# Performance work log

Measured on AMD Instinct MI355X. Metric: run time of the kernel, lower is better.

Reference implementation:

```python
import jax, jax.numpy as jnp
import numpy as np

K = 16            # neighbors
QUERY_CHUNK = 256 # SE is applied per chunk of this many query points (matches torch loop)
EPS = 1e-5        # BatchNorm eps (eval mode, running stats)


def bn(x, g, b, m, v):
    # eval-mode batchnorm over last axis (channel-last layout here)
    return (x - m) * (g / jnp.sqrt(v + EPS)) + b


def setup_inputs() -> dict:
    key = jax.random.key(0)
    ks = jax.random.split(key, 16)
    B, Cin, N = 4, 128, 4096
    H, Cout = 128, 256
    se_h = Cout // 4
    r = lambda k, s, sc=1.0: jax.random.normal(k, s, jnp.float32) * sc
    return dict(
        x=r(ks[0], (B, Cin, N)),
        W_edge=r(ks[1], (H, 2 * Cin), 0.05),          # edge_mlp conv2d 1x1
        bn1_g=jnp.ones((H,), jnp.float32), bn1_b=jnp.zeros((H,), jnp.float32),
        bn1_m=r(ks[2], (H,), 0.1), bn1_v=jax.random.uniform(ks[3], (H,), jnp.float32) + 0.5,
        w_att=r(ks[4], (H,), 0.1),                     # att_conv (1,H,1,1)
        W_fuse=r(ks[5], (Cout, H), 0.05),              # fuse conv1d
        bn2_g=jnp.ones((Cout,), jnp.float32), bn2_b=jnp.zeros((Cout,), jnp.float32),
        bn2_m=r(ks[6], (Cout,), 0.1), bn2_v=jax.random.uniform(ks[7], (Cout,), jnp.float32) + 0.5,
        fc1_w=r(ks[8], (se_h, Cout), 0.05), fc1_b=jnp.zeros((se_h,), jnp.float32),
        fc2_w=r(ks[9], (Cout, se_h), 0.05), fc2_b=jnp.zeros((Cout,), jnp.float32),
        W_res=r(ks[10], (Cout, Cin), 0.05),            # res_conv conv1d (in!=out)
        bn3_g=jnp.ones((Cout,), jnp.float32), bn3_b=jnp.zeros((Cout,), jnp.float32),
        bn3_m=r(ks[11], (Cout,), 0.1), bn3_v=jax.random.uniform(ks[12], (Cout,), jnp.float32) + 0.5,
    )


def reference(x, W_edge, bn1_g, bn1_b, bn1_m, bn1_v, w_att,
              W_fuse, bn2_g, bn2_b, bn2_m, bn2_v,
              fc1_w, fc1_b, fc2_w, fc2_b,
              W_res, bn3_g, bn3_b, bn3_m, bn3_v):
    B, Cin, N = x.shape
    x_t = jnp.swapaxes(x, 1, 2)  # (B,N,Cin)

    # KNN on features (dynamic=False -> knn on x.transpose); squared euclidean
    # has the same ordering as torch.cdist(p=2).
    sq = jnp.sum(x_t * x_t, axis=-1)                               # (B,N)
    d2 = sq[:, :, None] + sq[:, None, :] - 2.0 * jnp.einsum('bnc,bmc->bnm', x_t, x_t)
    _, idx = jax.lax.top_k(-d2, K)                                  # (B,N,K) smallest dists

    neigh = jax.vmap(lambda p, i: p[i])(x_t, idx)                   # (B,N,K,Cin)
    center = jnp.broadcast_to(x_t[:, :, None, :], neigh.shape)      # (B,N,K,Cin)
    edge = jnp.concatenate([neigh - center, center], axis=-1)       # (B,N,K,2Cin)

    # edge_mlp: 1x1 conv + BN + ReLU
    h = jax.nn.relu(bn(jnp.einsum('bnkc,hc->bnkh', edge, W_edge),
                       bn1_g, bn1_b, bn1_m, bn1_v))                 # (B,N,K,H)

    # attention over neighbors
    att = jax.nn.softmax(jnp.einsum('bnkh,h->bnk', h, w_att), axis=-1)
    agg = jnp.einsum('bnkh,bnk->bnh', h, att)                       # (B,N,H)

    # fuse conv1d + BN + ReLU
    out = jax.nn.relu(bn(jnp.einsum('bnh,oh->bno', agg, W_fuse),
                         bn2_g, bn2_b, bn2_m, bn2_v))               # (B,N,Cout)

    # SE channel attention, applied per query chunk (matches torch loop semantics)
    Cout = out.shape[-1]
    nc = N // QUERY_CHUNK
    oc = out.reshape(B, nc, QUERY_CHUNK, Cout)
    s = oc.mean(axis=2)                                             # (B,nc,Cout)
    s = jax.nn.relu(jnp.einsum('bmc,hc->bmh', s, fc1_w) + fc1_b)
    s = jax.nn.sigmoid(jnp.einsum('bmh,ch->bmc', s, fc2_w) + fc2_b)
    out = (oc * s[:, :, None, :]).reshape(B, N, Cout)

    # residual projection (in_channels != out_channels)
    res = bn(jnp.einsum('bnc,oc->bno', x_t, W_res), bn3_g, bn3_b, bn3_m, bn3_v)
    out = out + res
    return jnp.swapaxes(out, 1, 2)                                  # (B,Cout,N)
```

## Files before the change

### kernel.cpp

```cpp
#include <hip/hip_runtime.h>
#include <cstddef>

typedef __bf16 bf16;
typedef __bf16 bf16x8 __attribute__((ext_vector_type(8)));
typedef float  f32x4  __attribute__((ext_vector_type(4)));
typedef unsigned short u16;
typedef unsigned long long u64;

#define MFMA16x16(a, b, c) __builtin_amdgcn_mfma_f32_16x16x32_bf16((a), (b), (c), 0, 0, 0)

namespace {
constexpr int BB   = 4;
constexpr int CIN  = 128;
constexpr int NPT  = 4096;
constexpr int KNBR = 16;
constexpr int HED  = 128;
constexpr int COUT = 256;
}

__device__ __forceinline__ double mk_keyd(float d, unsigned mlo ) {
  const u64 k = ((u64)__float_as_uint(d) << 32) | mlo;
  return __longlong_as_double((long long)k);
}
__device__ __forceinline__ int key_idx(double kd) {
  return (int)((__double_as_longlong(kd) >> 20) & 0xFFF);
}

__device__ __forceinline__ void sort16d(double* k) {
  #pragma unroll
  for (int sz = 2; sz <= 16; sz <<= 1) {
    #pragma unroll
    for (int st = sz >> 1; st > 0; st >>= 1) {
      #pragma unroll
      for (int i = 0; i < 16; ++i) {
        const int j = i ^ st;
        if (j > i) {
          const bool up = ((i & sz) == 0);
          const double a = k[i], c = k[j];
          const double lo = fmin(a, c), hi = fmax(a, c);
          k[i] = up ? lo : hi;
          k[j] = up ? hi : lo;
        }
      }
    }
  }
}

__device__ __forceinline__ void merge16d(double* R, const double* B) {
  double t[16];
  #pragma unroll
  for (int i = 0; i < 16; ++i) t[i] = fmin(R[i], B[15 - i]);
  #pragma unroll
  for (int st = 8; st > 0; st >>= 1) {
    #pragma unroll
    for (int i = 0; i < 16; ++i) {
      const int j = i ^ st;
      if (j > i) {
        const double a = t[i], c = t[j];
        t[i] = fmin(a, c);
        t[j] = fmax(a, c);
      }
    }
  }
  #pragma unroll
  for (int i = 0; i < 16; ++i) R[i] = t[i];
}

__device__ __forceinline__ void shfl_merge16d(double* R, int mask) {
  double B[16];
  #pragma unroll
  for (int i = 0; i < 16; ++i) B[i] = __shfl_xor(R[i], mask, 64);
  merge16d(R, B);
}

__global__ __launch_bounds__(256) void k_wconv(const float* __restrict__ We,
                                               const float* __restrict__ Wf,
                                               const float* __restrict__ Wr,
                                               bf16* __restrict__ Web,
                                               bf16* __restrict__ Wfb,
                                               bf16* __restrict__ Wrb) {
  const int i = blockIdx.x * 256 + threadIdx.x;
  const int a = i >> 15;
  const int j = i & 32767;
  const float* src = (a == 0) ? We : (a == 1) ? Wf : Wr;
  bf16*        dst = (a == 0) ? Web : (a == 1) ? Wfb : Wrb;
  dst[j] = (bf16)src[j];
}

__global__ __launch_bounds__(256) void k_prep(const float* __restrict__ x,
                                              bf16* __restrict__ xh,
                                              bf16* __restrict__ xl,
                                              float* __restrict__ sq) {
  __shared__ __attribute__((aligned(16))) bf16 th[64][136];
  __shared__ __attribute__((aligned(16))) bf16 tl[64][136];
  __shared__ float sqp[4][64];
  const int tid = threadIdx.x;
  const int b   = blockIdx.x >> 6;
  const int n0  = (blockIdx.x & 63) << 6;
  const int nl  = tid & 63;
  const int cg  = tid >> 6;
  const float* xb = x + (size_t)b * CIN * NPT;
  float acc = 0.f;
  #pragma unroll
  for (int rep = 0; rep < 32; ++rep) {
    const int c = rep * 4 + cg;
    const float v = xb[(size_t)c * NPT + n0 + nl];
    const bf16 h = (bf16)v;
    const bf16 l = (bf16)(v - (float)h);
    acc += v * v;
    th[nl][c] = h;
    tl[nl][c] = l;
  }
  sqp[cg][nl] = acc;
  __syncthreads();
  bf16* xho = xh + ((size_t)b * NPT + n0) * CIN;
  bf16* xlo = xl + ((size_t)b * NPT + n0) * CIN;
  #pragma unroll
  for (int rep = 0; rep < 32; ++rep) {
    const int e = rep * 256 + tid;
    const int r = e >> 7;
    const int c = e & 127;
    xho[(size_t)r * CIN + c] = th[r][c];
    xlo[(size_t)r * CIN + c] = tl[r][c];
  }
  if (tid < 64) {
    sq[b * NPT + n0 + tid] = sqp[0][tid] + sqp[1][tid] + sqp[2][tid] + sqp[3][tid];
  }
}

__global__ __launch_bounds__(256, 2) void k_knn(const bf16* __restrict__ xh,
                                                const bf16* __restrict__ xl,
                                                const float* __restrict__ sq,
                                                int* __restrict__ knn_idx) {
  __shared__ double Lk[32][66];
  const int tid  = threadIdx.x;
  const int w    = tid >> 6;
  const int lane = tid & 63;
  const int col  = lane & 15;
  const int quad = lane >> 4;
  const int b    = blockIdx.x >> 7;
  const int q0   = (blockIdx.x & 127) << 5;
  const bf16*  xhb = xh + (size_t)b * NPT * CIN;
  const bf16*  xlb = xl + (size_t)b * NPT * CIN;
  const float* sqb = sq + b * NPT;

  bf16x8 qh[2][4], ql[2][4];
  float sqn[2];
  #pragma unroll
  for (int t = 0; t < 2; ++t) {
    const bf16* qrh = xhb + (size_t)(q0 + t * 16 + col) * CIN + quad * 8;
    const bf16* qrl = xlb + (size_t)(q0 + t * 16 + col) * CIN + quad * 8;
    #pragma unroll
    for (int ks = 0; ks < 4; ++ks) {
      qh[t][ks] = *(const bf16x8*)(qrh + ks * 32);
      ql[t][ks] = *(const bf16x8*)(qrl + ks * 32);
    }
    sqn[t] = sqb[q0 + t * 16 + col];
  }

  const double INF = __builtin_inf();
  double R0[16], R1[16];
  #pragma unroll
  for (int i = 0; i < 16; ++i) { R0[i] = INF; R1[i] = INF; }

  const int cbase = w << 10;
  for (int mt = 0; mt < 16; ++mt) {
    const int m0 = cbase + (mt << 6);
    double k0[16], k1[16];
    #pragma unroll
    for (int cb = 0; cb < 4; ++cb) {
      const bf16* crh = xhb + (size_t)(m0 + cb * 16 + col) * CIN + quad * 8;
      const bf16* crl = xlb + (size_t)(m0 + cb * 16 + col) * CIN + quad * 8;
      f32x4 a0 = {0.f, 0.f, 0.f, 0.f};
      f32x4 a1 = {0.f, 0.f, 0.f, 0.f};
      #pragma unroll
      for (int ks = 0; ks < 4; ++ks) {
        const bf16x8 ch_ = *(const bf16x8*)(crh + ks * 32);
        const bf16x8 cl_ = *(const bf16x8*)(crl + ks * 32);
        a0 = MFMA16x16(cl_, qh[0][ks], a0);
        a0 = MFMA16x16(ch_, ql[0][ks], a0);
        a0 = MFMA16x16(ch_, qh[0][ks], a0);
        a1 = MFMA16x16(cl_, qh[1][ks], a1);
        a1 = MFMA16x16(ch_, ql[1][ks], a1);
        a1 = MFMA16x16(ch_, qh[1][ks], a1);
      }
      const f32x4 sqm = *(const f32x4*)(sqb + m0 + cb * 16 + quad * 4);
      const unsigned mlo0 = (unsigned)(m0 + cb * 16 + quad * 4) << 20;
      #pragma unroll
      for (int r = 0; r < 4; ++r) {
        k0[cb * 4 + r] = mk_keyd((sqn[0] + sqm[r]) - 2.0f * a0[r], mlo0 + ((unsigned)r << 20));
        k1[cb * 4 + r] = mk_keyd((sqn[1] + sqm[r]) - 2.0f * a1[r], mlo0 + ((unsigned)r << 20));
      }
    }
    sort16d(k0); merge16d(R0, k0);
    sort16d(k1); merge16d(R1, k1);
  }

  shfl_merge16d(R0, 16);
  shfl_merge16d(R0, 32);
  shfl_merge16d(R1, 16);
  shfl_merge16d(R1, 32);

  if (quad == 0) {
    #pragma unroll
    for (int i = 0; i < 16; ++i) {
      Lk[col][w * 16 + i]        = R0[i];
      Lk[16 | col][w * 16 + i]   = R1[i];
    }
  }
  __syncthreads();

  if (tid < 64) {
    const int q = tid >> 1;
    const int j = tid & 1;
    double A[16], Bv[16];
    #pragma unroll
    for (int i = 0; i < 16; ++i) {
      A[i]  = Lk[q][(2 * j) * 16 + i];
      Bv[i] = Lk[q][(2 * j + 1) * 16 + i];
    }
    merge16d(A, Bv);
    #pragma unroll
    for (int i = 0; i < 16; ++i) Lk[q][j * 16 + i] = A[i];
  }
  __syncthreads();
  if (tid < 32) {
    double A[16], Bv[16];
    #pragma unroll
    for (int i = 0; i < 16; ++i) {
      A[i]  = Lk[tid][i];
      Bv[i] = Lk[tid][16 + i];
    }
    merge16d(A, Bv);
    int* op = knn_idx + (size_t)(b * NPT + q0 + tid) * KNBR;
    #pragma unroll
    for (int i = 0; i < 16; ++i) op[i] = key_idx(A[i]);
  }
}

__global__ __launch_bounds__(256) void k_edge(const bf16* __restrict__ xh,
                                              const bf16* __restrict__ xl,
                                              const int* __restrict__ knn_idx,
                                              const bf16* __restrict__ We,
                                              const float* __restrict__ g1, const float* __restrict__ b1,
                                              const float* __restrict__ m1, const float* __restrict__ v1,
                                              const float* __restrict__ watt,
                                              bf16* __restrict__ agg) {
  __shared__ __attribute__((aligned(16))) bf16 Ew[4][16][264];
  __shared__ float s1[HED], t1[HED], wat[HED];
  const int tid  = threadIdx.x;
  const int w    = tid >> 6;
  const int lane = tid & 63;
  const int col  = lane & 15;
  const int quad = lane >> 4;
  if (tid < HED) {
    const float ss = g1[tid] / sqrtf(v1[tid] + 1e-5f);
    s1[tid] = ss;
    t1[tid] = b1[tid] - m1[tid] * ss;
    wat[tid] = watt[tid];
  }
  __syncthreads();
  const int gw = blockIdx.x * 4 + w;
  for (int it = 0; it < 4; ++it) {
    const int p = gw * 4 + it;
    const int b = p >> 12;
    const int n = p & 4095;
    const bf16* xhb = xh + (size_t)b * NPT * CIN;
    const bf16* xlb = xl + (size_t)b * NPT * CIN;
    const int my = knn_idx[(size_t)p * KNBR + col];
    const int m  = __shfl(my, lane >> 2);
    const int sub = lane & 3;
    const int kn  = lane >> 2;
    const bf16* nh = xhb + (size_t)m * CIN + sub * 32;
    const bf16* nl_ = xlb + (size_t)m * CIN + sub * 32;
    const bf16* ch = xhb + (size_t)n * CIN + sub * 32;
    const bf16* cl = xlb + (size_t)n * CIN + sub * 32;
    #pragma unroll
    for (int j = 0; j < 4; ++j) {
      const bf16x8 nhv = *(const bf16x8*)(nh + j * 8);
      const bf16x8 nlv = *(const bf16x8*)(nl_ + j * 8);
      const bf16x8 chv = *(const bf16x8*)(ch + j * 8);
      const bf16x8 clv = *(const bf16x8*)(cl + j * 8);
      bf16x8 dv, cv;
      #pragma unroll
      for (int e = 0; e < 8; ++e) {
        const float nf = (float)nhv[e] + (float)nlv[e];
        const float cf = (float)chv[e] + (float)clv[e];
        dv[e] = (bf16)(nf - cf);
        cv[e] = (bf16)cf;
      }
      *(bf16x8*)&Ew[w][kn][sub * 32 + j * 8]       = dv;
      *(bf16x8*)&Ew[w][kn][128 + sub * 32 + j * 8] = cv;
    }
    const f32x4 zero4 = {0.f, 0.f, 0.f, 0.f};
    f32x4 acc[8];
    #pragma unroll
    for (int hb = 0; hb < 8; ++hb) acc[hb] = zero4;
    #pragma unroll
    for (int ks = 0; ks < 8; ++ks) {
      const bf16x8 af = *(const bf16x8*)&Ew[w][col][ks * 32 + quad * 8];
      #pragma unroll
      for (int hb = 0; hb < 8; ++hb) {
        const bf16x8 bfv = *(const bf16x8*)(We + (size_t)(hb * 16 + col) * 256 + ks * 32 + quad * 8);
        acc[hb] = MFMA16x16(af, bfv, acc[hb]);
      }
    }
    float h[8][4];
    float lg[4] = {0.f, 0.f, 0.f, 0.f};
    #pragma unroll
    for (int hb = 0; hb < 8; ++hb) {
      const int hc = hb * 16 + col;
      const float ss = s1[hc], tt = t1[hc], ww = wat[hc];
      #pragma unroll
      for (int r = 0; r < 4; ++r) {
        const float hv = fmaxf(acc[hb][r] * ss + tt, 0.f);
        h[hb][r] = hv;
        lg[r] += hv * ww;
      }
    }
    #pragma unroll
    for (int r = 0; r < 4; ++r) {
      float vv = lg[r];
      vv += __shfl_xor(vv, 1);
      vv += __shfl_xor(vv, 2);
      vv += __shfl_xor(vv, 4);
      vv += __shfl_xor(vv, 8);
      lg[r] = vv;
    }
    float mx = fmaxf(fmaxf(lg[0], lg[1]), fmaxf(lg[2], lg[3]));
    mx = fmaxf(mx, __shfl_xor(mx, 16));
    mx = fmaxf(mx, __shfl_xor(mx, 32));
    float ex[4];
    float sm = 0.f;
    #pragma unroll
    for (int r = 0; r < 4; ++r) { ex[r] = expf(lg[r] - mx); sm += ex[r]; }
    sm += __shfl_xor(sm, 16);
    sm += __shfl_xor(sm, 32);
    const float inv = 1.0f / sm;
    float ag[8];
    #pragma unroll
    for (int hb = 0; hb < 8; ++hb) {
      float a = h[hb][0] * ex[0] + h[hb][1] * ex[1] + h[hb][2] * ex[2] + h[hb][3] * ex[3];
      a += __shfl_xor(a, 16);
      a += __shfl_xor(a, 32);
      ag[hb] = a * inv;
    }
    if (quad == 0) {
      bf16* ao = agg + (size_t)p * HED;
      #pragma unroll
      for (int hb = 0; hb < 8; ++hb) ao[hb * 16 + col] = (bf16)ag[hb];
    }
  }
}

__global__ __launch_bounds__(256) void k_fuse(const bf16* __restrict__ agg,
                                              const bf16* __restrict__ Wf,
                                              const float* __restrict__ g2, const float* __restrict__ b2,
                                              const float* __restrict__ m2, const float* __restrict__ v2,
                                              bf16* __restrict__ outp) {
  const int tid  = threadIdx.x;
  const int w    = tid >> 6;
  const int lane = tid & 63;
  const int col  = lane & 15;
  const int quad = lane >> 4;
  const int p0   = (blockIdx.x * 4 + w) * 16;
  bf16x8 afr[4];
  const bf16* arow = agg + (size_t)(p0 + col) * HED + quad * 8;
  #pragma unroll
  for (int ks = 0; ks < 4; ++ks) afr[ks] = *(const bf16x8*)(arow + ks * 32);
  #pragma unroll
  for (int ob = 0; ob < 16; ++ob) {
    f32x4 acc = {0.f, 0.f, 0.f, 0.f};
    const bf16* brow = Wf + (size_t)(ob * 16 + col) * HED + quad * 8;
    #pragma unroll
    for (int ks = 0; ks < 4; ++ks)
      acc = MFMA16x16(afr[ks], *(const bf16x8*)(brow + ks * 32), acc);
    const int o = ob * 16 + col;
    const float ss = g2[o] / sqrtf(v2[o] + 1e-5f);
    const float tt = b2[o] - m2[o] * ss;
    #pragma unroll
    for (int r = 0; r < 4; ++r) {
      outp[(size_t)(p0 + quad * 4 + r) * COUT + o] = (bf16)fmaxf(acc[r] * ss + tt, 0.f);
    }
  }
}

__global__ __launch_bounds__(256) void k_se(const bf16* __restrict__ outp,
                                            const float* __restrict__ f1w, const float* __restrict__ f1b,
                                            const float* __restrict__ f2w, const float* __restrict__ f2b,
                                            float* __restrict__ sse) {
  __shared__ float mean_s[COUT];
  __shared__ float h1[64];
  const int bc  = blockIdx.x;
  const int tid = threadIdx.x;
  const bf16* base = outp + (size_t)bc * 256 * COUT;
  float s = 0.f;
  for (int p2 = 0; p2 < 256; ++p2) s += (float)base[(size_t)p2 * COUT + tid];
  mean_s[tid] = s * (1.0f / 256.0f);
  __syncthreads();
  if (tid < 64) {
    float a = f1b[tid];
    for (int c = 0; c < COUT; ++c) a += f1w[tid * COUT + c] * mean_s[c];
    h1[tid] = fmaxf(a, 0.f);
  }
  __syncthreads();
  float a = f2b[tid];
  #pragma unroll
  for (int j = 0; j < 64; ++j) a += f2w[tid * 64 + j] * h1[j];
  sse[(size_t)bc * COUT + tid] = 1.0f / (1.0f + expf(-a));
}

__global__ __launch_bounds__(256) void k_final(const bf16* __restrict__ xh,
                                               const bf16* __restrict__ Wr,
                                               const float* __restrict__ g3, const float* __restrict__ b3,
                                               const float* __restrict__ m3, const float* __restrict__ v3,
                                               const bf16* __restrict__ outp,
                                               const float* __restrict__ sse,
                                               float* __restrict__ out) {
  const int tid  = threadIdx.x;
  const int w    = tid >> 6;
  const int lane = tid & 63;
  const int col  = lane & 15;
  const int quad = lane >> 4;
  const int p0   = (blockIdx.x * 4 + w) * 16;
  const int b    = p0 >> 12;
  const int n0l  = p0 & 4095;
  bf16x8 afr[4];
  const bf16* arow = xh + (size_t)(p0 + col) * CIN + quad * 8;
  #pragma unroll
  for (int ks = 0; ks < 4; ++ks) afr[ks] = *(const bf16x8*)(arow + ks * 32);
  const float* scb = sse + (size_t)(b * 16 + (n0l >> 8)) * COUT;
  #pragma unroll
  for (int ob = 0; ob < 16; ++ob) {
    f32x4 acc = {0.f, 0.f, 0.f, 0.f};
    const bf16* brow = Wr + (size_t)(ob * 16 + col) * CIN + quad * 8;
    #pragma unroll
    for (int ks = 0; ks < 4; ++ks)
      acc = MFMA16x16(afr[ks], *(const bf16x8*)(brow + ks * 32), acc);
    const int o = ob * 16 + col;
    const float ss = g3[o] / sqrtf(v3[o] + 1e-5f);
    const float tt = b3[o] - m3[o] * ss;
    const float sc = scb[o];
    f32x4 pk;
    #pragma unroll
    for (int r = 0; r < 4; ++r) {
      const float res = acc[r] * ss + tt;
      pk[r] = (float)outp[(size_t)(p0 + quad * 4 + r) * COUT + o] * sc + res;
    }
    float* op = out + (size_t)(b * COUT + o) * NPT + n0l + quad * 4;
    *(f32x4*)op = pk;
  }
}

extern "C" void kernel_launch(void* const* d_in, const int* in_sizes, int n_in,
                              void* d_out, int out_size, void* d_ws, size_t ws_size,
                              hipStream_t stream) {
  (void)in_sizes; (void)n_in; (void)out_size; (void)ws_size;
  const float* x    = (const float*)d_in[0];
  const float* We   = (const float*)d_in[1];
  const float* g1   = (const float*)d_in[2];
  const float* b1   = (const float*)d_in[3];
  const float* m1   = (const float*)d_in[4];
  const float* v1   = (const float*)d_in[5];
  const float* watt = (const float*)d_in[6];
  const float* Wf   = (const float*)d_in[7];
  const float* g2   = (const float*)d_in[8];
  const float* b2   = (const float*)d_in[9];
  const float* m2   = (const float*)d_in[10];
  const float* v2   = (const float*)d_in[11];
  const float* f1w  = (const float*)d_in[12];
  const float* f1b  = (const float*)d_in[13];
  const float* f2w  = (const float*)d_in[14];
  const float* f2b  = (const float*)d_in[15];
  const float* Wr   = (const float*)d_in[16];
  const float* g3   = (const float*)d_in[17];
  const float* b3   = (const float*)d_in[18];
  const float* m3   = (const float*)d_in[19];
  const float* v3   = (const float*)d_in[20];

  char* ws = (char*)d_ws;
  size_t off = 0;
  bf16*  xth  = (bf16*)(ws + off);  off += (size_t)BB * NPT * CIN * 2;
  bf16*  xtl  = (bf16*)(ws + off);  off += (size_t)BB * NPT * CIN * 2;
  float* sq   = (float*)(ws + off); off += (size_t)BB * NPT * 4;
  int*   idxp = (int*)(ws + off);   off += (size_t)BB * NPT * KNBR * 4;
  bf16*  aggp = (bf16*)(ws + off);  off += (size_t)BB * NPT * HED * 2;
  bf16*  outp = (bf16*)(ws + off);  off += (size_t)BB * NPT * COUT * 2;
  float* ssep = (float*)(ws + off); off += (size_t)BB * 16 * COUT * 4;
  bf16*  Web  = (bf16*)(ws + off);  off += (size_t)HED * 2 * CIN * 2;
  bf16*  Wfb  = (bf16*)(ws + off);  off += (size_t)COUT * HED * 2;
  bf16*  Wrb  = (bf16*)(ws + off);  off += (size_t)COUT * CIN * 2;

  float* out = (float*)d_out;

  k_wconv<<<384, 256, 0, stream>>>(We, Wf, Wr, Web, Wfb, Wrb);
  k_prep<<<256, 256, 0, stream>>>(x, xth, xtl, sq);
  k_knn<<<512, 256, 0, stream>>>(xth, xtl, sq, idxp);
  k_edge<<<1024, 256, 0, stream>>>(xth, xtl, idxp, Web, g1, b1, m1, v1, watt, aggp);
  k_fuse<<<256, 256, 0, stream>>>(aggp, Wfb, g2, b2, m2, v2, outp);
  k_se<<<64, 256, 0, stream>>>(outp, f1w, f1b, f2w, f2b, ssep);
  k_final<<<256, 256, 0, stream>>>(xth, Wrb, g3, b3, m3, v3, outp, ssep, out);
}
```

Baseline: 398.6 us.

## Split KNN query tiles across twice as many waves to cut register pressure

Each wave of the KNN kernel now handles one 16-query tile instead of two. The block grows to 512 threads, so 8 waves cover 2 query tiles times 4 candidate ranges. This halves the per-thread top-16 and key register arrays so more waves can be resident. The cost is that each candidate row is loaded from global or L2 by two waves instead of once. The in-block final merge still uses the same Lk layout.

Result: slower. 503.8 us (+26.4%).

```diff
diff --git a/kernel.cpp b/kernel.cpp
--- a/kernel.cpp
+++ b/kernel.cpp
@@ -128,7 +128,7 @@
   }
 }
 
-__global__ __launch_bounds__(256, 2) void k_knn(const bf16* __restrict__ xh,
+__global__ __launch_bounds__(512, 4) void k_knn(const bf16* __restrict__ xh,
                                                 const bf16* __restrict__ xl,
                                                 const float* __restrict__ sq,
                                                 int* __restrict__ knn_idx) {
@@ -138,75 +138,65 @@
   const int lane = tid & 63;
   const int col  = lane & 15;
   const int quad = lane >> 4;
+  const int t    = w & 1;
+  const int crng = w >> 1;
   const int b    = blockIdx.x >> 7;
   const int q0   = (blockIdx.x & 127) << 5;
   const bf16*  xhb = xh + (size_t)b * NPT * CIN;
   const bf16*  xlb = xl + (size_t)b * NPT * CIN;
   const float* sqb = sq + b * NPT;
 
-  bf16x8 qh[2][4], ql[2][4];
-  float sqn[2];
-  #pragma unroll
-  for (int t = 0; t < 2; ++t) {
+  bf16x8 qh[4], ql[4];
+  {
     const bf16* qrh = xhb + (size_t)(q0 + t * 16 + col) * CIN + quad * 8;
     const bf16* qrl = xlb + (size_t)(q0 + t * 16 + col) * CIN + quad * 8;
     #pragma unroll
     for (int ks = 0; ks < 4; ++ks) {
-      qh[t][ks] = *(const bf16x8*)(qrh + ks * 32);
-      ql[t][ks] = *(const bf16x8*)(qrl + ks * 32);
-    }
-    sqn[t] = sqb[q0 + t * 16 + col];
-  }
+      qh[ks] = *(const bf16x8*)(qrh + ks * 32);
+      ql[ks] = *(const bf16x8*)(qrl + ks * 32);
+    }
+  }
+  const float sqn = sqb[q0 + t * 16 + col];
 
   const double INF = __builtin_inf();
-  double R0[16], R1[16];
-  #pragma unroll
-  for (int i = 0; i < 16; ++i) { R0[i] = INF; R1[i] = INF; }
-
-  const int cbase = w << 10;
+  double R[16];
+  #pragma unroll
+  for (int i = 0; i < 16; ++i) R[i] = INF;
+
+  const int cbase = crng << 10;
   for (int mt = 0; mt < 16; ++mt) {
     const int m0 = cbase + (mt << 6);
-    double k0[16], k1[16];
+    double k[16];
     #pragma unroll
     for (int cb = 0; cb < 4; ++cb) {
       const bf16* crh = xhb + (size_t)(m0 + cb * 16 + col) * CIN + quad * 8;
       const bf16* crl = xlb + (size_t)(m0 + cb * 16 + col) * CIN + quad * 8;
       f32x4 a0 = {0.f, 0.f, 0.f, 0.f};
-      f32x4 a1 = {0.f, 0.f, 0.f, 0.f};
       #pragma unroll
       for (int ks = 0; ks < 4; ++ks) {
         const bf16x8 ch_ = *(const bf16x8*)(crh + ks * 32);
         const bf16x8 cl_ = *(const bf16x8*)(crl + ks * 32);
-        a0 = MFMA16x16(cl_, qh[0][ks], a0);
-        a0 = MFMA16x16(ch_, ql[0][ks], a0);
-        a0 = MFMA16x16(ch_, qh[0][ks], a0);
-        a1 = MFMA16x16(cl_, qh[1][ks], a1);
-        a1 = MFMA16x16(ch_, ql[1][ks], a1);
-        a1 = MFMA16x16(ch_, qh[1][ks], a1);
+        a0 = MFMA16x16(cl_, qh[ks], a0);
+        a0 = MFMA16x16(ch_, ql[ks], a0);
+        a0 = MFMA16x16(ch_, qh[ks], a0);
       }
       const f32x4 sqm = *(const f32x4*)(sqb + m0 + cb * 16 + quad * 4);
       const unsigned mlo0 = (unsigned)(m0 + cb * 16 + quad * 4) << 20;
       #pragma unroll
       for (int r = 0; r < 4; ++r) {
-        k0[cb * 4 + r] = mk_keyd((sqn[0] + sqm[r]) - 2.0f * a0[r], mlo0 + ((unsigned)r << 20));
-        k1[cb * 4 + r] = mk_keyd((sqn[1] + sqm[r]) - 2.0f * a1[r], mlo0 + ((unsigned)r << 20));
-      }
-    }
-    sort16d(k0); merge16d(R0, k0);
-    sort16d(k1); merge16d(R1, k1);
-  }
-
-  shfl_merge16d(R0, 16);
-  shfl_merge16d(R0, 32);
-  shfl_merge16d(R1, 16);
-  shfl_merge16d(R1, 32);
+        k[cb * 4 + r] = mk_keyd((sqn + sqm[r]) - 2.0f * a0[r], mlo0 + ((unsigned)r << 20));
+      }
+    }
+    sort16d(k);
+    merge16d(R, k);
+  }
+
+  shfl_merge16d(R, 16);
+  shfl_merge16d(R, 32);
 
   if (quad == 0) {
     #pragma unroll
-    for (int i = 0; i < 16; ++i) {
-      Lk[col][w * 16 + i]        = R0[i];
-      Lk[16 | col][w * 16 + i]   = R1[i];
-    }
+    for (int i = 0; i < 16; ++i) Lk[t * 16 + col][crng * 16 + i] = R[i];
   }
   __syncthreads();
 
@@ -495,7 +485,7 @@
 
   k_wconv<<<384, 256, 0, stream>>>(We, Wf, Wr, Web, Wfb, Wrb);
   k_prep<<<256, 256, 0, stream>>>(x, xth, xtl, sq);
-  k_knn<<<512, 256, 0, stream>>>(xth, xtl, sq, idxp);
+  k_knn<<<512, 512, 0, stream>>>(xth, xtl, sq, idxp);
   k_edge<<<1024, 256, 0, stream>>>(xth, xtl, idxp, Web, g1, b1, m1, v1, watt, aggp);
   k_fuse<<<256, 256, 0, stream>>>(aggp, Wfb, g2, b2, m2, v2, outp);
   k_se<<<64, 256, 0, stream>>>(outp, f1w, f1b, f2w, f2b, ssep);
```

## Increase grid parallelism in edge, fuse, final kernels and split SE reduction

Applied to the files above, without the earlier changes.

Each wave in the edge kernel now handles one point instead of looping over four, so that kernel launches 4096 blocks. The fuse and final kernels split the output channels across four blocks each and launch 1024 blocks. The SE mean is split into a partial-sum kernel over 256 blocks plus a small reduce-and-MLP kernel. The aim is more waves in flight on a GPU with many CUs, at the cost of extra launches, repeated per-block setup (BN params, A-fragment loads) and an additional partial-sum buffer.

Result: slower. 421.8 us (+5.8%).

```diff
diff --git a/kernel.cpp b/kernel.cpp
--- a/kernel.cpp
+++ b/kernel.cpp
@@ -260,96 +260,93 @@
     wat[tid] = watt[tid];
   }
   __syncthreads();
-  const int gw = blockIdx.x * 4 + w;
-  for (int it = 0; it < 4; ++it) {
-    const int p = gw * 4 + it;
-    const int b = p >> 12;
-    const int n = p & 4095;
-    const bf16* xhb = xh + (size_t)b * NPT * CIN;
-    const bf16* xlb = xl + (size_t)b * NPT * CIN;
-    const int my = knn_idx[(size_t)p * KNBR + col];
-    const int m  = __shfl(my, lane >> 2);
-    const int sub = lane & 3;
-    const int kn  = lane >> 2;
-    const bf16* nh = xhb + (size_t)m * CIN + sub * 32;
-    const bf16* nl_ = xlb + (size_t)m * CIN + sub * 32;
-    const bf16* ch = xhb + (size_t)n * CIN + sub * 32;
-    const bf16* cl = xlb + (size_t)n * CIN + sub * 32;
-    #pragma unroll
-    for (int j = 0; j < 4; ++j) {
-      const bf16x8 nhv = *(const bf16x8*)(nh + j * 8);
-      const bf16x8 nlv = *(const bf16x8*)(nl_ + j * 8);
-      const bf16x8 chv = *(const bf16x8*)(ch + j * 8);
-      const bf16x8 clv = *(const bf16x8*)(cl + j * 8);
-      bf16x8 dv, cv;
-      #pragma unroll
-      for (int e = 0; e < 8; ++e) {
-        const float nf = (float)nhv[e] + (float)nlv[e];
-        const float cf = (float)chv[e] + (float)clv[e];
-        dv[e] = (bf16)(nf - cf);
-        cv[e] = (bf16)cf;
-      }
-      *(bf16x8*)&Ew[w][kn][sub * 32 + j * 8]       = dv;
-      *(bf16x8*)&Ew[w][kn][128 + sub * 32 + j * 8] = cv;
-    }
-    const f32x4 zero4 = {0.f, 0.f, 0.f, 0.f};
-    f32x4 acc[8];
-    #pragma unroll
-    for (int hb = 0; hb < 8; ++hb) acc[hb] = zero4;
-    #pragma unroll
-    for (int ks = 0; ks < 8; ++ks) {
-      const bf16x8 af = *(const bf16x8*)&Ew[w][col][ks * 32 + quad * 8];
-      #pragma unroll
-      for (int hb = 0; hb < 8; ++hb) {
-        const bf16x8 bfv = *(const bf16x8*)(We + (size_t)(hb * 16 + col) * 256 + ks * 32 + quad * 8);
-        acc[hb] = MFMA16x16(af, bfv, acc[hb]);
-      }
-    }
-    float h[8][4];
-    float lg[4] = {0.f, 0.f, 0.f, 0.f};
+  const int p = blockIdx.x * 4 + w;
+  const int b = p >> 12;
+  const int n = p & 4095;
+  const bf16* xhb = xh + (size_t)b * NPT * CIN;
+  const bf16* xlb = xl + (size_t)b * NPT * CIN;
+  const int my = knn_idx[(size_t)p * KNBR + col];
+  const int m  = __shfl(my, lane >> 2);
+  const int sub = lane & 3;
+  const int kn  = lane >> 2;
+  const bf16* nh = xhb + (size_t)m * CIN + sub * 32;
+  const bf16* nl_ = xlb + (size_t)m * CIN + sub * 32;
+  const bf16* ch = xhb + (size_t)n * CIN + sub * 32;
+  const bf16* cl = xlb + (size_t)n * CIN + sub * 32;
+  #pragma unroll
+  for (int j = 0; j < 4; ++j) {
+    const bf16x8 nhv = *(const bf16x8*)(nh + j * 8);
+    const bf16x8 nlv = *(const bf16x8*)(nl_ + j * 8);
+    const bf16x8 chv = *(const bf16x8*)(ch + j * 8);
+    const bf16x8 clv = *(const bf16x8*)(cl + j * 8);
+    bf16x8 dv, cv;
+    #pragma unroll
+    for (int e = 0; e < 8; ++e) {
+      const float nf = (float)nhv[e] + (float)nlv[e];
+      const float cf = (float)chv[e] + (float)clv[e];
+      dv[e] = (bf16)(nf - cf);
+      cv[e] = (bf16)cf;
+    }
+    *(bf16x8*)&Ew[w][kn][sub * 32 + j * 8]       = dv;
+    *(bf16x8*)&Ew[w][kn][128 + sub * 32 + j * 8] = cv;
+  }
+  const f32x4 zero4 = {0.f, 0.f, 0.f, 0.f};
+  f32x4 acc[8];
+  #pragma unroll
+  for (int hb = 0; hb < 8; ++hb) acc[hb] = zero4;
+  #pragma unroll
+  for (int ks = 0; ks < 8; ++ks) {
+    const bf16x8 af = *(const bf16x8*)&Ew[w][col][ks * 32 + quad * 8];
     #pragma unroll
     for (int hb = 0; hb < 8; ++hb) {
-      const int hc = hb * 16 + col;
-      const float ss = s1[hc], tt = t1[hc], ww = wat[hc];
-      #pragma unroll
-      for (int r = 0; r < 4; ++r) {
-        const float hv = fmaxf(acc[hb][r] * ss + tt, 0.f);
-        h[hb][r] = hv;
-        lg[r] += hv * ww;
-      }
-    }
+      const bf16x8 bfv = *(const bf16x8*)(We + (size_t)(hb * 16 + col) * 256 + ks * 32 + quad * 8);
+      acc[hb] = MFMA16x16(af, bfv, acc[hb]);
+    }
+  }
+  float h[8][4];
+  float lg[4] = {0.f, 0.f, 0.f, 0.f};
+  #pragma unroll
+  for (int hb = 0; hb < 8; ++hb) {
+    const int hc = hb * 16 + col;
+    const float ss = s1[hc], tt = t1[hc], ww = wat[hc];
     #pragma unroll
     for (int r = 0; r < 4; ++r) {
-      float vv = lg[r];
-      vv += __shfl_xor(vv, 1);
-      vv += __shfl_xor(vv, 2);
-      vv += __shfl_xor(vv, 4);
-      vv += __shfl_xor(vv, 8);
-      lg[r] = vv;
-    }
-    float mx = fmaxf(fmaxf(lg[0], lg[1]), fmaxf(lg[2], lg[3]));
-    mx = fmaxf(mx, __shfl_xor(mx, 16));
-    mx = fmaxf(mx, __shfl_xor(mx, 32));
-    float ex[4];
-    float sm = 0.f;
-    #pragma unroll
-    for (int r = 0; r < 4; ++r) { ex[r] = expf(lg[r] - mx); sm += ex[r]; }
-    sm += __shfl_xor(sm, 16);
-    sm += __shfl_xor(sm, 32);
-    const float inv = 1.0f / sm;
-    float ag[8];
-    #pragma unroll
-    for (int hb = 0; hb < 8; ++hb) {
-      float a = h[hb][0] * ex[0] + h[hb][1] * ex[1] + h[hb][2] * ex[2] + h[hb][3] * ex[3];
-      a += __shfl_xor(a, 16);
-      a += __shfl_xor(a, 32);
-      ag[hb] = a * inv;
-    }
-    if (quad == 0) {
-      bf16* ao = agg + (size_t)p * HED;
-      #pragma unroll
-      for (int hb = 0; hb < 8; ++hb) ao[hb * 16 + col] = (bf16)ag[hb];
-    }
+      const float hv = fmaxf(acc[hb][r] * ss + tt, 0.f);
+      h[hb][r] = hv;
+      lg[r] += hv * ww;
+    }
+  }
+  #pragma unroll
+  for (int r = 0; r < 4; ++r) {
+    float vv = lg[r];
+    vv += __shfl_xor(vv, 1);
+    vv += __shfl_xor(vv, 2);
+    vv += __shfl_xor(vv, 4);
+    vv += __shfl_xor(vv, 8);
+    lg[r] = vv;
+  }
+  float mx = fmaxf(fmaxf(lg[0], lg[1]), fmaxf(lg[2], lg[3]));
+  mx = fmaxf(mx, __shfl_xor(mx, 16));
+  mx = fmaxf(mx, __shfl_xor(mx, 32));
+  float ex[4];
+  float sm = 0.f;
+  #pragma unroll
+  for (int r = 0; r < 4; ++r) { ex[r] = expf(lg[r] - mx); sm += ex[r]; }
+  sm += __shfl_xor(sm, 16);
+  sm += __shfl_xor(sm, 32);
+  const float inv = 1.0f / sm;
+  float ag[8];
+  #pragma unroll
+  for (int hb = 0; hb < 8; ++hb) {
+    float a = h[hb][0] * ex[0] + h[hb][1] * ex[1] + h[hb][2] * ex[2] + h[hb][3] * ex[3];
+    a += __shfl_xor(a, 16);
+    a += __shfl_xor(a, 32);
+    ag[hb] = a * inv;
+  }
+  if (quad == 0) {
+    bf16* ao = agg + (size_t)p * HED;
+    #pragma unroll
+    for (int hb = 0; hb < 8; ++hb) ao[hb * 16 + col] = (bf16)ag[hb];
   }
 }
 
@@ -363,13 +360,16 @@
   const int lane = tid & 63;
   const int col  = lane & 15;
   const int quad = lane >> 4;
-  const int p0   = (blockIdx.x * 4 + w) * 16;
+  const int pb   = blockIdx.x >> 2;
+  const int obq  = blockIdx.x & 3;
+  const int p0   = (pb * 4 + w) * 16;
   bf16x8 afr[4];
   const bf16* arow = agg + (size_t)(p0 + col) * HED + quad * 8;
   #pragma unroll
   for (int ks = 0; ks < 4; ++ks) afr[ks] = *(const bf16x8*)(arow + ks * 32);
   #pragma unroll
-  for (int ob = 0; ob < 16; ++ob) {
+  for (int i = 0; i < 4; ++i) {
+    const int ob = obq * 4 + i;
     f32x4 acc = {0.f, 0.f, 0.f, 0.f};
     const bf16* brow = Wf + (size_t)(ob * 16 + col) * HED + quad * 8;
     #pragma unroll
@@ -385,18 +385,26 @@
   }
 }
 
-__global__ __launch_bounds__(256) void k_se(const bf16* __restrict__ outp,
-                                            const float* __restrict__ f1w, const float* __restrict__ f1b,
-                                            const float* __restrict__ f2w, const float* __restrict__ f2b,
-                                            float* __restrict__ sse) {
+__global__ __launch_bounds__(256) void k_se1(const bf16* __restrict__ outp,
+                                             float* __restrict__ part) {
+  const int blk = blockIdx.x;
+  const int tid = threadIdx.x;
+  const bf16* base = outp + ((size_t)(blk >> 2) * 256 + (size_t)(blk & 3) * 64) * COUT;
+  float s = 0.f;
+  for (int p2 = 0; p2 < 64; ++p2) s += (float)base[(size_t)p2 * COUT + tid];
+  part[(size_t)blk * COUT + tid] = s;
+}
+
+__global__ __launch_bounds__(256) void k_se2(const float* __restrict__ part,
+                                             const float* __restrict__ f1w, const float* __restrict__ f1b,
+                                             const float* __restrict__ f2w, const float* __restrict__ f2b,
+                                             float* __restrict__ sse) {
   __shared__ float mean_s[COUT];
   __shared__ float h1[64];
   const int bc  = blockIdx.x;
   const int tid = threadIdx.x;
-  const bf16* base = outp + (size_t)bc * 256 * COUT;
-  float s = 0.f;
-  for (int p2 = 0; p2 < 256; ++p2) s += (float)base[(size_t)p2 * COUT + tid];
-  mean_s[tid] = s * (1.0f / 256.0f);
+  const float* pb = part + (size_t)bc * 4 * COUT;
+  mean_s[tid] = (pb[tid] + pb[COUT + tid] + pb[2 * COUT + tid] + pb[3 * COUT + tid]) * (1.0f / 256.0f);
   __syncthreads();
   if (tid < 64) {
     float a = f1b[tid];
@@ -422,7 +430,9 @@
   const int lane = tid & 63;
   const int col  = lane & 15;
   const int quad = lane >> 4;
-  const int p0   = (blockIdx.x * 4 + w) * 16;
+  const int pb   = blockIdx.x >> 2;
+  const int obq  = blockIdx.x & 3;
+  const int p0   = (pb * 4 + w) * 16;
   const int b    = p0 >> 12;
   const int n0l  = p0 & 4095;
   bf16x8 afr[4];
@@ -431,7 +441,8 @@
   for (int ks = 0; ks < 4; ++ks) afr[ks] = *(const bf16x8*)(arow + ks * 32);
   const float* scb = sse + (size_t)(b * 16 + (n0l >> 8)) * COUT;
   #pragma unroll
-  for (int ob = 0; ob < 16; ++ob) {
+  for (int i = 0; i < 4; ++i) {
+    const int ob = obq * 4 + i;
     f32x4 acc = {0.f, 0.f, 0.f, 0.f};
     const bf16* brow = Wr + (size_t)(ob * 16 + col) * CIN + quad * 8;
     #pragma unroll
@@ -487,6 +498,7 @@
   bf16*  aggp = (bf16*)(ws + off);  off += (size_t)BB * NPT * HED * 2;
   bf16*  outp = (bf16*)(ws + off);  off += (size_t)BB * NPT * COUT * 2;
   float* ssep = (float*)(ws + off); off += (size_t)BB * 16 * COUT * 4;
+  float* partp= (float*)(ws + off); off += (size_t)256 * COUT * 4;
   bf16*  Web  = (bf16*)(ws + off);  off += (size_t)HED * 2 * CIN * 2;
   bf16*  Wfb  = (bf16*)(ws + off);  off += (size_t)COUT * HED * 2;
   bf16*  Wrb  = (bf16*)(ws + off);  off += (size_t)COUT * CIN * 2;
@@ -496,8 +508,9 @@
   k_wconv<<<384, 256, 0, stream>>>(We, Wf, Wr, Web, Wfb, Wrb);
   k_prep<<<256, 256, 0, stream>>>(x, xth, xtl, sq);
   k_knn<<<512, 256, 0, stream>>>(xth, xtl, sq, idxp);
-  k_edge<<<1024, 256, 0, stream>>>(xth, xtl, idxp, Web, g1, b1, m1, v1, watt, aggp);
-  k_fuse<<<256, 256, 0, stream>>>(aggp, Wfb, g2, b2, m2, v2, outp);
-  k_se<<<64, 256, 0, stream>>>(outp, f1w, f1b, f2w, f2b, ssep);
-  k_final<<<256, 256, 0, stream>>>(xth, Wrb, g3, b3, m3, v3, outp, ssep, out);
-}
+  k_edge<<<4096, 256, 0, stream>>>(xth, xtl, idxp, Web, g1, b1, m1, v1, watt, aggp);
+  k_fuse<<<1024, 256, 0, stream>>>(aggp, Wfb, g2, b2, m2, v2, outp);
+  k_se1<<<256, 256, 0, stream>>>(outp, partp);
+  k_se2<<<64, 256, 0, stream>>>(partp, f1w, f1b, f2w, f2b, ssep);
+  k_final<<<1024, 256, 0, stream>>>(xth, Wrb, g3, b3, m3, v3, outp, ssep, out);
+}
```
